# Performance work log

Measured on AMD Instinct MI355X. Metric: run time of the kernel, lower is better.

The kernel has to match this reference:

```python
import jax, jax.numpy as jnp
import numpy as np

NUM_HEADS = 8

def setup_inputs() -> dict:
    key = jax.random.key(0)
    k1, k2, k3, k4 = jax.random.split(key, 4)
    B, N, S, C = 16, 256, 4096, 512
    return {
        "query": jax.random.normal(k1, (B, N, C), dtype=jnp.float32),
        "key": jax.random.normal(k2, (B, S, C), dtype=jnp.float32),
        "Wq": jax.random.normal(k3, (C, C), dtype=jnp.float32) * (C ** -0.5),
        "Wk": jax.random.normal(k4, (C, C), dtype=jnp.float32) * (C ** -0.5),
    }

def reference(query, key, Wq, Wk):
    B, N, C = query.shape
    S = key.shape[1]
    H = NUM_HEADS
    hd = C // H
    scale = hd ** -0.5
    # value = key (v_proj is Identity, value defaults to key)
    q = (query @ Wq).reshape(B, N, H, hd)   # b n h c
    k = (key @ Wk).reshape(B, S, H, hd)     # b s h c
    raw_attn = jnp.einsum('bnhc,bshc->bhns', q, k) * scale  # [B,H,N,S]
    # softmax over the QUERY axis (dim=-2), non-standard
    attn = jax.nn.softmax(raw_attn, axis=-2)
    # clamp-normalize over token axis; divisor is detached in the original
    div = jnp.clip(jnp.sum(attn, axis=-1, keepdims=True), 1.0, None)
    attn = attn / jax.lax.stop_gradient(div)
    # attn_drop has p=0.0 -> identity
    v = key.reshape(B, S, H, hd)
    out = jnp.einsum('bhns,bshc->bnhc', attn, v).reshape(B, N, C)
    # out_style = attn @ key_heads; since value == key this equals out
    out_style = out
    return out, out_style
```

## Files before the change

kernel.cpp:

```cpp
#include <hip/hip_runtime.h>
#include <hip/hip_bf16.h>


typedef __attribute__((ext_vector_type(8))) short bf16x8;
typedef __attribute__((ext_vector_type(4))) float f32x4;
typedef unsigned int u32;

__device__ __forceinline__ unsigned short f2bf(float f) {
  union { __hip_bfloat16 h; unsigned short u; } cv;
  cv.h = __float2bfloat16(f);
  return cv.u;
}

__device__ __forceinline__ u32 pkbf(float a, float b) {
  union { __hip_bfloat162 h; u32 u; } cv;
  cv.h = __float22bfloat162_rn(float2{a, b});
  return cv.u;
}

__global__ __launch_bounds__(256) void prep_w(const float* __restrict__ Wq,
                                              const float* __restrict__ Wk,
                                              unsigned short* __restrict__ WtQ,
                                              unsigned short* __restrict__ WtK) {
  __shared__ float tile[64][65];
  const int blk = blockIdx.x;
  const float* W = (blk & 1) ? Wk : Wq;
  unsigned short* Wt = (blk & 1) ? WtK : WtQ;
  const int tb = blk >> 1;
  const int k0 = (tb >> 3) * 64, n0 = (tb & 7) * 64;
  const int t = threadIdx.x;
  const int row = t >> 4, col4 = (t & 15) * 4;
#pragma unroll
  for (int i = 0; i < 4; ++i) {
    int r = i * 16 + row;
    float4 v = *reinterpret_cast<const float4*>(&W[(size_t)(k0 + r) * 512 + n0 + col4]);
    tile[r][col4 + 0] = v.x; tile[r][col4 + 1] = v.y;
    tile[r][col4 + 2] = v.z; tile[r][col4 + 3] = v.w;
  }
  __syncthreads();
#pragma unroll
  for (int i = 0; i < 4; ++i) {
    int r = i * 16 + row;
    short4 s;
    s.x = (short)f2bf(tile[col4 + 0][r]);
    s.y = (short)f2bf(tile[col4 + 1][r]);
    s.z = (short)f2bf(tile[col4 + 2][r]);
    s.w = (short)f2bf(tile[col4 + 3][r]);
    *reinterpret_cast<short4*>(&Wt[(size_t)(n0 + r) * 512 + k0 + col4]) = s;
  }
}

__global__ __launch_bounds__(256, 2) void gemm_xw(const float* __restrict__ X,
                                                  const unsigned short* __restrict__ Wt,
                                                  __hip_bfloat16* __restrict__ Y) {
  __shared__ unsigned short As[2][128 * 64];
  __shared__ unsigned short Bs[2][128 * 64];
  const int t = threadIdx.x;
  const int wave = t >> 6, lane = t & 63, l15 = lane & 15, quad = lane >> 4;

  const int nwg = gridDim.x * gridDim.y;
  const int d = blockIdx.y * gridDim.x + blockIdx.x;
  const int tile = (d & 7) * (nwg >> 3) + (d >> 3);
  const int n0 = (tile & 3) * 128, m0 = (tile >> 2) * 128;

  const int wm = (wave >> 1) * 64, wn = (wave & 1) * 64;
  const int cr = t >> 3, cc = t & 7;

  const float* aB = X + (size_t)m0 * 512;
  const unsigned short* bB = Wt + (size_t)n0 * 512;

  f32x4 acc[4][4];
#pragma unroll
  for (int i = 0; i < 4; ++i)
#pragma unroll
    for (int j = 0; j < 4; ++j) { f32x4 z = {0.f, 0.f, 0.f, 0.f}; acc[i][j] = z; }

  float4 fA[2][4][2];
  uint4  fB[2][4];

#define GEMM_ISSUE(kt) do {                                                          \
    const int S_ = (kt) & 1; const int kk_ = (kt) * 64;                              \
    _Pragma("unroll")                                                                \
    for (int i_ = 0; i_ < 4; ++i_) {                                                 \
      const float* ap_ = aB + (size_t)(i_ * 32 + cr) * 512 + kk_ + cc * 8;           \
      fA[S_][i_][0] = *reinterpret_cast<const float4*>(ap_);                         \
      fA[S_][i_][1] = *reinterpret_cast<const float4*>(ap_ + 4);                     \
      fB[S_][i_] = *reinterpret_cast<const uint4*>(                                  \
          bB + (size_t)(i_ * 32 + cr) * 512 + kk_ + cc * 8);                         \
    }                                                                                \
  } while (0)

#define GEMM_STAGE(kt) do {                                                          \
    const int S_ = (kt) & 1;                                                         \
    _Pragma("unroll")                                                                \
    for (int i_ = 0; i_ < 4; ++i_) {                                                 \
      int r_ = i_ * 32 + cr;                                                         \
      uint4 w_;                                                                      \
      w_.x = pkbf(fA[S_][i_][0].x, fA[S_][i_][0].y);                                 \
      w_.y = pkbf(fA[S_][i_][0].z, fA[S_][i_][0].w);                                 \
      w_.z = pkbf(fA[S_][i_][1].x, fA[S_][i_][1].y);                                 \
      w_.w = pkbf(fA[S_][i_][1].z, fA[S_][i_][1].w);                                 \
      int off_ = r_ * 64 + ((cc ^ (r_ & 7)) << 3);                                   \
      *reinterpret_cast<uint4*>(&As[S_][off_]) = w_;                                 \
      *reinterpret_cast<uint4*>(&Bs[S_][off_]) = fB[S_][i_];                         \
    }                                                                                \
  } while (0)

#define GEMM_COMPUTE(kt) do {                                                        \
    const int S_ = (kt) & 1;                                                         \
    _Pragma("unroll")                                                                \
    for (int x_ = 0; x_ < 2; ++x_) {                                                 \
      bf16x8 a_[4], b_[4];                                                           \
      _Pragma("unroll")                                                              \
      for (int i_ = 0; i_ < 4; ++i_) {                                               \
        int ra_ = wm + 16 * i_ + l15;                                                \
        a_[i_] = *reinterpret_cast<const bf16x8*>(                                   \
            &As[S_][ra_ * 64 + (((x_ * 4 + quad) ^ (ra_ & 7)) << 3)]);               \
      }                                                                              \
      _Pragma("unroll")                                                              \
      for (int j_ = 0; j_ < 4; ++j_) {                                               \
        int rb_ = wn + 16 * j_ + l15;                                                \
        b_[j_] = *reinterpret_cast<const bf16x8*>(                                   \
            &Bs[S_][rb_ * 64 + (((x_ * 4 + quad) ^ (rb_ & 7)) << 3)]);               \
      }                                                                              \
      _Pragma("unroll")                                                              \
      for (int i_ = 0; i_ < 4; ++i_)                                                 \
        _Pragma("unroll")                                                            \
        for (int j_ = 0; j_ < 4; ++j_)                                               \
          acc[i_][j_] =                                                              \
              __builtin_amdgcn_mfma_f32_16x16x32_bf16(a_[i_], b_[j_], acc[i_][j_],   \
                                                      0, 0, 0);                      \
    }                                                                                \
  } while (0)

  GEMM_ISSUE(0);
  GEMM_ISSUE(1);
  GEMM_STAGE(0);
  asm volatile("s_waitcnt lgkmcnt(0)" ::: "memory");
  __builtin_amdgcn_sched_barrier(0);
  __builtin_amdgcn_s_barrier();
  __builtin_amdgcn_sched_barrier(0);

#pragma unroll
  for (int it = 0; it < 8; ++it) {
    if (it < 6) GEMM_ISSUE(it + 2);
    __builtin_amdgcn_sched_barrier(0);
    GEMM_COMPUTE(it);
    if (it < 7) {
      __builtin_amdgcn_sched_barrier(0);
      GEMM_STAGE(it + 1);
      asm volatile("s_waitcnt lgkmcnt(0)" ::: "memory");
      __builtin_amdgcn_sched_barrier(0);
      __builtin_amdgcn_s_barrier();
      __builtin_amdgcn_sched_barrier(0);
    }
  }

#undef GEMM_ISSUE
#undef GEMM_STAGE
#undef GEMM_COMPUTE

#pragma unroll
  for (int i = 0; i < 4; ++i)
#pragma unroll
    for (int j = 0; j < 4; ++j)
#pragma unroll
      for (int r = 0; r < 4; ++r) {
        int m = m0 + wm + 16 * i + 4 * quad + r;
        int n = n0 + wn + 16 * j + l15;
        Y[(size_t)m * 512 + n] = __float2bfloat16(acc[i][j][r]);
      }
}

__global__ __launch_bounds__(512, 2) void attn_kernel(const __hip_bfloat16* __restrict__ qg,
                                                      const __hip_bfloat16* __restrict__ kg,
                                                      const float* __restrict__ keyg,
                                                      float* __restrict__ accg,
                                                      float* __restrict__ rsg) {
  __shared__ unsigned short qs[256 * 64];
  __shared__ unsigned short vs[64 * 128];
  __shared__ unsigned short pst[256 * 128];

  const int t = threadIdx.x;
  const int wave = t >> 6, lane = t & 63, l15 = lane & 15, quad = lane >> 4;
  const int blk = blockIdx.x, chunk = blk & 1, bh = blk >> 1, b = bh >> 3, h = bh & 7;
  const int l7 = l15 & 7;

  {
    const unsigned short* qbase = (const unsigned short*)qg + (size_t)(b * 256) * 512 + h * 64;
#pragma unroll
    for (int i = 0; i < 4; ++i) {
      int lin = i * 512 + t;
      int n = lin >> 3, cc = lin & 7, phys = cc ^ (n & 7);
      bf16x8 v = *reinterpret_cast<const bf16x8*>(qbase + (size_t)n * 512 + cc * 8);
      *reinterpret_cast<bf16x8*>(&qs[n * 64 + phys * 8]) = v;
    }
  }

  const unsigned short* kbase = (const unsigned short*)kg + (size_t)(b * 4096 + chunk * 2048) * 512 + h * 64;
  const float* vbase = keyg + (size_t)(b * 4096 + chunk * 2048) * 512 + h * 64;

  bf16x8 kc0 = *reinterpret_cast<const bf16x8*>(kbase + (size_t)(16 * wave + l15) * 512 + quad * 8);
  bf16x8 kc1 = *reinterpret_cast<const bf16x8*>(kbase + (size_t)(16 * wave + l15) * 512 + 32 + quad * 8);
  float vbuf[16];
#pragma unroll
  for (int half = 0; half < 2; ++half) {
    int sc = wave + 8 * half;
#pragma unroll
    for (int j = 0; j < 8; ++j)
      vbuf[half * 8 + j] = vbase[(size_t)(sc * 8 + j) * 512 + lane];
  }

  union { bf16x8 f; int w[4]; } ones_u;
  ones_u.w[0] = 0x3F803F80; ones_u.w[1] = 0x3F803F80;
  ones_u.w[2] = 0x3F803F80; ones_u.w[3] = 0x3F803F80;
  const bf16x8 ones = ones_u.f;

  f32x4 oacc[2][4], rsacc[2];
#pragma unroll
  for (int i = 0; i < 2; ++i) {
    f32x4 z = {0.f, 0.f, 0.f, 0.f};
    rsacc[i] = z;
#pragma unroll
    for (int j = 0; j < 4; ++j) oacc[i][j] = z;
  }

  __syncthreads();

  for (int it = 0; it < 16; ++it) {
    f32x4 L[16];
#pragma unroll
    for (int jt = 0; jt < 16; ++jt) { f32x4 z = {0.f, 0.f, 0.f, 0.f}; L[jt] = z; }
#pragma unroll
    for (int x = 0; x < 2; ++x) {
      bf16x8 kf = x ? kc1 : kc0;
#pragma unroll
      for (int jt = 0; jt < 16; ++jt) {
        bf16x8 bq = *reinterpret_cast<const bf16x8*>(
            &qs[(16 * jt + l15) * 64 + ((4 * x + quad) ^ l7) * 8]);
        L[jt] = __builtin_amdgcn_mfma_f32_16x16x32_bf16(kf, bq, L[jt], 0, 0, 0);
      }
    }

    const int nit = (it < 15) ? it + 1 : 15;
    kc0 = *reinterpret_cast<const bf16x8*>(kbase + (size_t)(nit * 128 + 16 * wave + l15) * 512 + quad * 8);
    kc1 = *reinterpret_cast<const bf16x8*>(kbase + (size_t)(nit * 128 + 16 * wave + l15) * 512 + 32 + quad * 8);

    float cs0 = 0.f, cs1 = 0.f, cs2 = 0.f, cs3 = 0.f;
#pragma unroll
    for (int jt = 0; jt < 16; ++jt) {
      float e0 = __expf(L[jt][0] * 0.125f);
      float e1 = __expf(L[jt][1] * 0.125f);
      float e2 = __expf(L[jt][2] * 0.125f);
      float e3 = __expf(L[jt][3] * 0.125f);
      L[jt][0] = e0; L[jt][1] = e1; L[jt][2] = e2; L[jt][3] = e3;
      cs0 += e0; cs1 += e1; cs2 += e2; cs3 += e3;
    }
#pragma unroll
    for (int m = 1; m <= 8; m <<= 1) {
      cs0 += __shfl_xor(cs0, m);
      cs1 += __shfl_xor(cs1, m);
      cs2 += __shfl_xor(cs2, m);
      cs3 += __shfl_xor(cs3, m);
    }
    const float ri0 = 1.0f / cs0, ri1 = 1.0f / cs1, ri2 = 1.0f / cs2, ri3 = 1.0f / cs3;

    __syncthreads();

#pragma unroll
    for (int half = 0; half < 2; ++half) {
      int sc = wave + 8 * half;
      uint4 w;
      w.x = pkbf(vbuf[half * 8 + 0], vbuf[half * 8 + 1]);
      w.y = pkbf(vbuf[half * 8 + 2], vbuf[half * 8 + 3]);
      w.z = pkbf(vbuf[half * 8 + 4], vbuf[half * 8 + 5]);
      w.w = pkbf(vbuf[half * 8 + 6], vbuf[half * 8 + 7]);
      *reinterpret_cast<uint4*>(&vs[lane * 128 + (sc ^ (lane & 7)) * 8]) = w;
    }

    {
      const int scw = 2 * wave + (quad >> 1);
      const int half8 = (quad & 1) * 4;
#pragma unroll
      for (int jt = 0; jt < 16; ++jt) {
        uint2 w;
        w.x = pkbf(L[jt][0] * ri0, L[jt][1] * ri1);
        w.y = pkbf(L[jt][2] * ri2, L[jt][3] * ri3);
        int row = 16 * jt + l15;
        *reinterpret_cast<uint2*>(&pst[row * 128 + ((scw ^ l7) * 8) + half8]) = w;
      }
    }

    __syncthreads();

#pragma unroll
    for (int half = 0; half < 2; ++half) {
      int sc = wave + 8 * half;
#pragma unroll
      for (int j = 0; j < 8; ++j)
        vbuf[half * 8 + j] = vbase[(size_t)(nit * 128 + sc * 8 + j) * 512 + lane];
    }

#pragma unroll
    for (int kc = 0; kc < 4; ++kc) {
      bf16x8 bv[4];
#pragma unroll
      for (int jc = 0; jc < 4; ++jc)
        bv[jc] = *reinterpret_cast<const bf16x8*>(
            &vs[(16 * jc + l15) * 128 + ((4 * kc + quad) ^ l7) * 8]);
#pragma unroll
      for (int jtl = 0; jtl < 2; ++jtl) {
        int rowp = 16 * (2 * wave + jtl) + l15;
        bf16x8 ap = *reinterpret_cast<const bf16x8*>(
            &pst[rowp * 128 + ((4 * kc + quad) ^ l7) * 8]);
#pragma unroll
        for (int jc = 0; jc < 4; ++jc)
          oacc[jtl][jc] = __builtin_amdgcn_mfma_f32_16x16x32_bf16(ap, bv[jc], oacc[jtl][jc], 0, 0, 0);
        rsacc[jtl] = __builtin_amdgcn_mfma_f32_16x16x32_bf16(ap, ones, rsacc[jtl], 0, 0, 0);
      }
    }
  }

  float* rsp = rsg + chunk * 32768 + bh * 256;
  if (l15 == 0) {
#pragma unroll
    for (int jtl = 0; jtl < 2; ++jtl)
#pragma unroll
      for (int r = 0; r < 4; ++r)
        rsp[16 * (2 * wave + jtl) + 4 * quad + r] = rsacc[jtl][r];
  }
  float* ap_ = accg + (size_t)chunk * 2097152 + (size_t)bh * 16384;
#pragma unroll
  for (int jtl = 0; jtl < 2; ++jtl)
#pragma unroll
    for (int jc = 0; jc < 4; ++jc)
#pragma unroll
      for (int r = 0; r < 4; ++r)
        ap_[(16 * (2 * wave + jtl) + 4 * quad + r) * 64 + 16 * jc + l15] = oacc[jtl][jc][r];
}

__global__ __launch_bounds__(256) void finalize(const float* __restrict__ acc,
                                                const float* __restrict__ rs,
                                                float* __restrict__ out) {
  int g = blockIdx.x * 256 + threadIdx.x;
  int c = (g & 15) * 4, n = (g >> 4) & 255, bh = g >> 12;
  int e = g * 4;
  float4 v0 = *reinterpret_cast<const float4*>(&acc[e]);
  float4 v1 = *reinterpret_cast<const float4*>(&acc[e + 2097152]);
  float r = rs[bh * 256 + n] + rs[32768 + bh * 256 + n];
  float inv = 1.0f / fmaxf(r, 1.0f);
  float4 o;
  o.x = (v0.x + v1.x) * inv; o.y = (v0.y + v1.y) * inv;
  o.z = (v0.z + v1.z) * inv; o.w = (v0.w + v1.w) * inv;
  int b = bh >> 3, h = bh & 7;
  size_t oi = ((size_t)(b * 256 + n)) * 512 + h * 64 + c;
  *reinterpret_cast<float4*>(&out[oi]) = o;
  *reinterpret_cast<float4*>(&out[oi + 2097152]) = o;
}

extern "C" void kernel_launch(void* const* d_in, const int* in_sizes, int n_in,
                              void* d_out, int out_size, void* d_ws, size_t ws_size,
                              hipStream_t stream) {
  const float* query = (const float*)d_in[0];
  const float* key   = (const float*)d_in[1];
  const float* Wq    = (const float*)d_in[2];
  const float* Wk    = (const float*)d_in[3];
  float* out = (float*)d_out;
  char* ws = (char*)d_ws;

  unsigned short* WtQ = (unsigned short*)(ws);
  unsigned short* WtK = (unsigned short*)(ws + 524288);
  __hip_bfloat16* qbf = (__hip_bfloat16*)(ws + 1048576);
  __hip_bfloat16* kbf = (__hip_bfloat16*)(ws + 5242880);
  float* accw = (float*)(ws + 72351744);
  float* rsw  = (float*)(ws + 89128960);

  prep_w<<<128, 256, 0, stream>>>(Wq, Wk, WtQ, WtK);
  gemm_xw<<<dim3(4, 32), 256, 0, stream>>>(query, WtQ, qbf);
  gemm_xw<<<dim3(4, 512), 256, 0, stream>>>(key, WtK, kbf);
  attn_kernel<<<256, 512, 0, stream>>>(qbf, kbf, key, accw, rsw);
  finalize<<<2048, 256, 0, stream>>>(accw, rsw, out);
}
```

Before: 339.1 us.

## Merge Q and K projection GEMMs into one launch with async LDS weight loads

Fuses the query and key projection GEMMs into a single grid, so tiles past index 2048 handle the query projection. The bf16 weight tile is now copied straight from global memory into LDS with global_load_lds, keeping the pre-swizzled XOR layout, rather than going through registers. The waitcnt schedule is reworked to track these async copies. This saves a kernel launch, fills the tail of the key GEMM with query work, and cuts register pressure and VALU/LDS-store work for the B operand, at the cost of more delicate vmcnt accounting.

```diff
diff --git a/kernel.cpp b/kernel.cpp
--- a/kernel.cpp
+++ b/kernel.cpp
@@ -16,6 +16,12 @@
   union { __hip_bfloat162 h; u32 u; } cv;
   cv.h = __float22bfloat162_rn(float2{a, b});
   return cv.u;
+}
+
+__device__ __forceinline__ void async_copy16(const void* gptr, void* lptr) {
+  __builtin_amdgcn_global_load_lds((const __attribute__((address_space(1))) u32*)gptr,
+                                   (__attribute__((address_space(3))) u32*)lptr,
+                                   16, 0, 0);
 }
 
 __global__ __launch_bounds__(256) void prep_w(const float* __restrict__ Wq,
@@ -50,9 +56,12 @@
   }
 }
 
-__global__ __launch_bounds__(256, 2) void gemm_xw(const float* __restrict__ X,
-                                                  const unsigned short* __restrict__ Wt,
-                                                  __hip_bfloat16* __restrict__ Y) {
+__global__ __launch_bounds__(256, 2) void gemm_xw(const float* __restrict__ Xk,
+                                                  const unsigned short* __restrict__ WtKp,
+                                                  __hip_bfloat16* __restrict__ Yk,
+                                                  const float* __restrict__ Xq,
+                                                  const unsigned short* __restrict__ WtQp,
+                                                  __hip_bfloat16* __restrict__ Yq) {
   __shared__ unsigned short As[2][128 * 64];
   __shared__ unsigned short Bs[2][128 * 64];
   const int t = threadIdx.x;
@@ -61,14 +70,16 @@
   const int nwg = gridDim.x * gridDim.y;
   const int d = blockIdx.y * gridDim.x + blockIdx.x;
   const int tile = (d & 7) * (nwg >> 3) + (d >> 3);
-  const int n0 = (tile & 3) * 128, m0 = (tile >> 2) * 128;
+
+  const float* X; const unsigned short* Wt; __hip_bfloat16* Y; int n0, m0;
+  if (tile < 2048) { X = Xk; Wt = WtKp; Y = Yk; n0 = (tile & 3) * 128; m0 = (tile >> 2) * 128; }
+  else { int u = tile - 2048; X = Xq; Wt = WtQp; Y = Yq; n0 = (u & 3) * 128; m0 = (u >> 2) * 128; }
 
   const int wm = (wave >> 1) * 64, wn = (wave & 1) * 64;
+  const int b_rl = lane >> 3;
+  const int b_cs = (lane & 7) ^ b_rl;
   const int cr = t >> 3, cc = t & 7;
 
-  const float* aB = X + (size_t)m0 * 512;
-  const unsigned short* bB = Wt + (size_t)n0 * 512;
-
   f32x4 acc[4][4];
 #pragma unroll
   for (int i = 0; i < 4; ++i)
@@ -76,37 +87,44 @@
     for (int j = 0; j < 4; ++j) { f32x4 z = {0.f, 0.f, 0.f, 0.f}; acc[i][j] = z; }
 
   float4 fA[2][4][2];
-  uint4  fB[2][4];
-
-#define GEMM_ISSUE(kt) do {                                                          \
+
+#define ISSUE_B(kt) do {                                                             \
     const int S_ = (kt) & 1; const int kk_ = (kt) * 64;                              \
+    const unsigned short* bB_ = Wt + (size_t)n0 * 512 + kk_;                         \
+    _Pragma("unroll")                                                                \
+    for (int o_ = 0; o_ < 4; ++o_) {                                                 \
+      int rg_ = wave * 4 + o_;                                                       \
+      async_copy16(bB_ + (size_t)(rg_ * 8 + b_rl) * 512 + b_cs * 8,                  \
+                   &Bs[S_][rg_ * 512]);                                              \
+    }                                                                                \
+  } while (0)
+
+#define ISSUE_A(kt) do {                                                             \
+    const int S_ = (kt) & 1; const int kk_ = (kt) * 64;                              \
+    const float* aB_ = X + (size_t)m0 * 512 + kk_;                                   \
     _Pragma("unroll")                                                                \
     for (int i_ = 0; i_ < 4; ++i_) {                                                 \
-      const float* ap_ = aB + (size_t)(i_ * 32 + cr) * 512 + kk_ + cc * 8;           \
-      fA[S_][i_][0] = *reinterpret_cast<const float4*>(ap_);                         \
-      fA[S_][i_][1] = *reinterpret_cast<const float4*>(ap_ + 4);                     \
-      fB[S_][i_] = *reinterpret_cast<const uint4*>(                                  \
-          bB + (size_t)(i_ * 32 + cr) * 512 + kk_ + cc * 8);                         \
+      const float* p_ = aB_ + (size_t)(i_ * 32 + cr) * 512 + cc * 8;                 \
+      fA[S_][i_][0] = *reinterpret_cast<const float4*>(p_);                          \
+      fA[S_][i_][1] = *reinterpret_cast<const float4*>(p_ + 4);                      \
     }                                                                                \
   } while (0)
 
-#define GEMM_STAGE(kt) do {                                                          \
+#define CVT_PUB(kt) do {                                                             \
     const int S_ = (kt) & 1;                                                         \
     _Pragma("unroll")                                                                \
     for (int i_ = 0; i_ < 4; ++i_) {                                                 \
-      int r_ = i_ * 32 + cr;                                                         \
       uint4 w_;                                                                      \
       w_.x = pkbf(fA[S_][i_][0].x, fA[S_][i_][0].y);                                 \
       w_.y = pkbf(fA[S_][i_][0].z, fA[S_][i_][0].w);                                 \
       w_.z = pkbf(fA[S_][i_][1].x, fA[S_][i_][1].y);                                 \
       w_.w = pkbf(fA[S_][i_][1].z, fA[S_][i_][1].w);                                 \
-      int off_ = r_ * 64 + ((cc ^ (r_ & 7)) << 3);                                   \
-      *reinterpret_cast<uint4*>(&As[S_][off_]) = w_;                                 \
-      *reinterpret_cast<uint4*>(&Bs[S_][off_]) = fB[S_][i_];                         \
+      int r_ = i_ * 32 + cr;                                                         \
+      *reinterpret_cast<uint4*>(&As[S_][r_ * 64 + ((cc ^ (r_ & 7)) << 3)]) = w_;     \
     }                                                                                \
   } while (0)
 
-#define GEMM_COMPUTE(kt) do {                                                        \
+#define COMPUTE(kt) do {                                                             \
     const int S_ = (kt) & 1;                                                         \
     _Pragma("unroll")                                                                \
     for (int x_ = 0; x_ < 2; ++x_) {                                                 \
@@ -133,9 +151,14 @@
     }                                                                                \
   } while (0)
 
-  GEMM_ISSUE(0);
-  GEMM_ISSUE(1);
-  GEMM_STAGE(0);
+  ISSUE_B(0);
+  __builtin_amdgcn_sched_barrier(0);
+  ISSUE_A(0);
+  __builtin_amdgcn_sched_barrier(0);
+  ISSUE_A(1);
+  __builtin_amdgcn_sched_barrier(0);
+  CVT_PUB(0);
+  asm volatile("s_waitcnt vmcnt(8)" ::: "memory");
   asm volatile("s_waitcnt lgkmcnt(0)" ::: "memory");
   __builtin_amdgcn_sched_barrier(0);
   __builtin_amdgcn_s_barrier();
@@ -143,12 +166,15 @@
 
 #pragma unroll
   for (int it = 0; it < 8; ++it) {
-    if (it < 6) GEMM_ISSUE(it + 2);
-    __builtin_amdgcn_sched_barrier(0);
-    GEMM_COMPUTE(it);
+    if (it < 7) { ISSUE_B(it + 1); __builtin_amdgcn_sched_barrier(0); }
+    if (it < 6) { ISSUE_A(it + 2); __builtin_amdgcn_sched_barrier(0); }
+
+    COMPUTE(it);
+
     if (it < 7) {
-      __builtin_amdgcn_sched_barrier(0);
-      GEMM_STAGE(it + 1);
+      CVT_PUB(it + 1);
+      if (it < 6) asm volatile("s_waitcnt vmcnt(8)" ::: "memory");
+      else        asm volatile("s_waitcnt vmcnt(0)" ::: "memory");
       asm volatile("s_waitcnt lgkmcnt(0)" ::: "memory");
       __builtin_amdgcn_sched_barrier(0);
       __builtin_amdgcn_s_barrier();
@@ -156,9 +182,10 @@
     }
   }
 
-#undef GEMM_ISSUE
-#undef GEMM_STAGE
-#undef GEMM_COMPUTE
+#undef ISSUE_B
+#undef ISSUE_A
+#undef CVT_PUB
+#undef COMPUTE
 
 #pragma unroll
   for (int i = 0; i < 4; ++i)
@@ -376,8 +403,7 @@
   float* rsw  = (float*)(ws + 89128960);
 
   prep_w<<<128, 256, 0, stream>>>(Wq, Wk, WtQ, WtK);
-  gemm_xw<<<dim3(4, 32), 256, 0, stream>>>(query, WtQ, qbf);
-  gemm_xw<<<dim3(4, 512), 256, 0, stream>>>(key, WtK, kbf);
+  gemm_xw<<<dim3(4, 544), 256, 0, stream>>>(key, WtK, kbf, query, WtQ, qbf);
   attn_kernel<<<256, 512, 0, stream>>>(qbf, kbf, key, accw, rsw);
   finalize<<<2048, 256, 0, stream>>>(accw, rsw, out);
 }
```

After: 320.6 us. -5.5%, faster.
